# Optimization experiments

Measured on AMD Instinct MI355X. Metric: run time of the kernel, lower is better.

The kernel has to match this reference:

```python
import jax, jax.numpy as jnp
import numpy as np

HIDDEN = 1408
HEADS = 16
HEAD_DIM = 88  # HIDDEN // HEADS
NUM_PATCHES = 576  # (336 // 14) ** 2
SEQ = NUM_PATCHES + 1  # +1 CLS token position in mllama4 rope cache
ROPE_BASE = 10000.0
SCALE = HEAD_DIM ** -0.5


def _rope_cos_sin():
    # Faithful to vLLM Llama4VisionRotaryEmbedding cos/sin cache.
    idx = np.arange(NUM_PATCHES, dtype=np.int64).reshape(NUM_PATCHES, 1)
    idx = np.concatenate([idx, idx[:1]], axis=0)
    idx[-1, -1] = -2  # CLS token id -> zero rotation
    n = int(np.sqrt(NUM_PATCHES))  # patches per side = 24
    fx = idx % n
    fy = idx // n
    rd = HEAD_DIM // 2  # rotary_dim = 44
    inv = 1.0 / ROPE_BASE ** (np.arange(0, rd, 2, dtype=np.float32) / rd)  # (22,)
    # repeat_interleave(2) then cat then [::2] == concat of the two 22-d halves
    freqs = np.concatenate(
        [(fx + 1)[..., None] * inv[None, None, :], (fy + 1)[..., None] * inv[None, None, :]],
        axis=-1,
    )  # (SEQ, 1, 44)
    freqs = np.where(idx.reshape(-1, 1, 1) < 0, 0.0, freqs).astype(np.float32)
    freqs = freqs.squeeze(1)  # (SEQ, 44)
    return jnp.asarray(np.cos(freqs)), jnp.asarray(np.sin(freqs))


_COS, _SIN = _rope_cos_sin()


def _apply_rope(x, cos, sin):
    # x: [B, S, H, D]; complex rotation over adjacent pairs (is_neox_style=False)
    B, S, H, D = x.shape
    xp = x.reshape(B, S, H, D // 2, 2)
    x0, x1 = xp[..., 0], xp[..., 1]
    c = cos[None, :, None, :]  # [1, S, 1, D//2]
    s = sin[None, :, None, :]
    out = jnp.stack([x0 * c - x1 * s, x0 * s + x1 * c], axis=-1)
    return out.reshape(B, S, H, D)


def setup_inputs() -> dict:
    key = jax.random.key(0)
    k1, k2, k3, k4, k5 = jax.random.split(key, 5)
    std = HIDDEN ** -0.5
    return {
        "hidden_states": jax.random.normal(k1, (32, SEQ, HIDDEN), dtype=jnp.float32),
        "w_qkv": jax.random.normal(k2, (HIDDEN, 3 * HIDDEN), dtype=jnp.float32) * std,
        "b_qkv": jax.random.normal(k3, (3 * HIDDEN,), dtype=jnp.float32) * 0.02,
        "w_o": jax.random.normal(k4, (HIDDEN, HIDDEN), dtype=jnp.float32) * std,
        "b_o": jax.random.normal(k5, (HIDDEN,), dtype=jnp.float32) * 0.02,
    }


def reference(hidden_states, w_qkv, b_qkv, w_o, b_o):
    B, S, _ = hidden_states.shape
    qkv = hidden_states @ w_qkv + b_qkv  # [B, S, 3*HIDDEN]
    q, k, v = jnp.split(qkv, 3, axis=-1)
    q = q.reshape(B, S, HEADS, HEAD_DIM)
    k = k.reshape(B, S, HEADS, HEAD_DIM)
    v = v.reshape(B, S, HEADS, HEAD_DIM)
    q = _apply_rope(q, _COS, _SIN)
    k = _apply_rope(k, _COS, _SIN)
    scores = jnp.einsum("bqhd,bkhd->bhqk", q, k) * SCALE
    probs = jax.nn.softmax(scores, axis=-1)
    attn = jnp.einsum("bhqk,bkhd->bqhd", probs, v).reshape(B, S, HIDDEN)
    return attn @ w_o + b_o
```

## Files before the change

### kernel.cpp

```cpp
#include <hip/hip_runtime.h>
#include <math.h>

#define HEADS    16
#define HEAD_DIM 88
#define SEQ      577
#define SEQV     640
#define HIDDEN   1408
#define NQKV     4224
#define NQKV_PAD 4352
#define NOUT_PAD 1536
#define RD       44
#define SCALE_F  0.1066003581778052f
#define MPAD_ROWS 18688
#define NKT      22
#define BUF_SH   32768

typedef __attribute__((ext_vector_type(8))) short bf16x8;
typedef __attribute__((ext_vector_type(4))) float f32x4;

__device__ __forceinline__ unsigned short f2bf(float x) {
    unsigned u = __float_as_uint(x);
    unsigned r = u + 0x7fff + ((u >> 16) & 1);
    return (unsigned short)(r >> 16);
}
__device__ __forceinline__ f32x4 fzero() {
    f32x4 z; z.x = 0.f; z.y = 0.f; z.z = 0.f; z.w = 0.f; return z;
}
__device__ __forceinline__ int xcd_swz(int flat, int nwg) {
    int q = nwg >> 3, r = nwg & 7;
    int x = flat & 7, j = flat >> 3;
    return (x < r ? x * (q + 1) : r * (q + 1) + (x - r) * q) + j;
}

__global__ void rope_precompute(float* __restrict__ cosb, float* __restrict__ sinb) {
    int s = blockIdx.x;
    int j = threadIdx.x;
    if (j >= RD) return;
    float c, sn;
    if (s == SEQ - 1) {
        c = 1.f; sn = 0.f;
    } else {
        int fx = s % 24, fy = s / 24;
        int p = (j < 22) ? j : j - 22;
        float inv = powf(10000.f, -(float)p / 22.f);
        float f = (float)((j < 22 ? fx : fy) + 1) * inv;
        c = cosf(f); sn = sinf(f);
    }
    cosb[s * RD + j] = c;
    sinb[s * RD + j] = sn;
}

__global__ void conv_hs(const float* __restrict__ in, unsigned short* __restrict__ out,
                        long nreal, long ntot) {
    long i = ((long)blockIdx.x * 256 + threadIdx.x) * 4;
    if (i >= ntot) return;
    ushort4 o;
    if (i < nreal) {
        float4 v = *(const float4*)(in + i);
        o = make_ushort4(f2bf(v.x), f2bf(v.y), f2bf(v.z), f2bf(v.w));
    } else {
        o = make_ushort4(0, 0, 0, 0);
    }
    *(ushort4*)(out + i) = o;
}

__global__ void conv_wT(const float* __restrict__ in, unsigned short* __restrict__ out,
                        int R, int Creal) {
    __shared__ float t[32][33];
    int bx = blockIdx.x * 32, by = blockIdx.y * 32;
    int tx = threadIdx.x & 31, ty = threadIdx.x >> 5;
    #pragma unroll
    for (int i = 0; i < 4; ++i) {
        int col = bx + tx;
        t[ty + i * 8][tx] = (col < Creal) ? in[(size_t)(by + ty + i * 8) * Creal + col] : 0.f;
    }
    __syncthreads();
    #pragma unroll
    for (int i = 0; i < 4; ++i)
        out[(size_t)(bx + ty + i * 8) * R + by + tx] = f2bf(t[tx][ty + i * 8]);
}

__device__ __forceinline__ void stage_half(const unsigned short* __restrict__ src,
                                           int kt, unsigned short* lds, int tid) {
    #pragma unroll
    for (int q = 0; q < 2; ++q) {
        int cf = tid + 512 * q;
        int r  = cf >> 3, c = cf & 7;
        int cg = c ^ (r & 7);
        __builtin_amdgcn_global_load_lds(
            (const __attribute__((address_space(1))) void*)(src + (size_t)r * HIDDEN + kt * 64 + cg * 8),
            (__attribute__((address_space(3))) void*)(lds + cf * 8),
            16, 0, 0);
    }
}

template<int N> __device__ __forceinline__ void vwait() {
    if constexpr (N >= 0)
        asm volatile("s_waitcnt vmcnt(%0)" :: "i"(N) : "memory");
}

template<int CBUF, int IH, int JH, bool STG, int SSIDE, int SHALF, int SBUF, int WAITN>
__device__ __forceinline__ void phase8(
    const unsigned short* __restrict__ wsrc, const unsigned short* __restrict__ hsrc,
    unsigned short* smem, int skt, int tid,
    int ww, int wh, int quad, int l15, f32x4 (&acc)[8][4])
{
    bf16x8 afr[4][2], bfr[2][2];
    #pragma unroll
    for (int i2 = 0; i2 < 4; ++i2)
        #pragma unroll
        for (int kk = 0; kk < 2; ++kk) {
            int r = ww * 64 + i2 * 16 + l15;
            afr[i2][kk] = *(const bf16x8*)(smem + CBUF * BUF_SH + IH * 8192
                          + r * 64 + (((kk * 4 + quad) ^ (r & 7)) << 3));
        }
    #pragma unroll
    for (int j2 = 0; j2 < 2; ++j2)
        #pragma unroll
        for (int kk = 0; kk < 2; ++kk) {
            int r = wh * 32 + j2 * 16 + l15;
            bfr[j2][kk] = *(const bf16x8*)(smem + CBUF * BUF_SH + 16384 + JH * 8192
                          + r * 64 + (((kk * 4 + quad) ^ (r & 7)) << 3));
        }
    if constexpr (STG) {
        const unsigned short* s = (SSIDE ? hsrc : wsrc) + (size_t)SHALF * 128 * HIDDEN;
        stage_half(s, skt, smem + SBUF * BUF_SH + (SSIDE ? 16384 : 0) + SHALF * 8192, tid);
    }
    __builtin_amdgcn_sched_barrier(0);
    __builtin_amdgcn_s_barrier();
    __builtin_amdgcn_sched_barrier(0);
    __builtin_amdgcn_s_setprio(1);
    #pragma unroll
    for (int i2 = 0; i2 < 4; ++i2)
        #pragma unroll
        for (int j2 = 0; j2 < 2; ++j2)
            #pragma unroll
            for (int kk = 0; kk < 2; ++kk)
                acc[IH * 4 + i2][JH * 2 + j2] = __builtin_amdgcn_mfma_f32_16x16x32_bf16(
                    afr[i2][kk], bfr[j2][kk], acc[IH * 4 + i2][JH * 2 + j2], 0, 0, 0);
    __builtin_amdgcn_s_setprio(0);
    __builtin_amdgcn_sched_barrier(0);
    vwait<WAITN>();
    __builtin_amdgcn_s_barrier();
    __builtin_amdgcn_sched_barrier(0);
}

__device__ __forceinline__ void gemm256_8ph(
    const unsigned short* __restrict__ wsrc, const unsigned short* __restrict__ hsrc,
    unsigned short* smem, int tid, f32x4 (&acc)[8][4])
{
    const int lane = tid & 63, w8 = tid >> 6;
    const int quad = lane >> 4, l15 = lane & 15;
    const int ww = w8 >> 2, wh = w8 & 3;

    stage_half(wsrc,                0, smem,                  tid);
    stage_half(hsrc,                0, smem + 16384,          tid);
    stage_half(wsrc + 128 * HIDDEN, 0, smem + 8192,           tid);
    stage_half(hsrc + 128 * HIDDEN, 0, smem + 24576,          tid);
    stage_half(wsrc,                1, smem + BUF_SH,         tid);
    stage_half(hsrc,                1, smem + BUF_SH + 16384, tid);
    asm volatile("s_waitcnt vmcnt(4)" ::: "memory");
    __builtin_amdgcn_s_barrier();
    __builtin_amdgcn_sched_barrier(0);

    for (int it = 0; it < 10; ++it) {
        int k1 = 2 * it + 1, k2 = 2 * it + 2, k3 = 2 * it + 3;
        phase8<0,0,0, true,0,1,1,  6>(wsrc, hsrc, smem, k1, tid, ww, wh, quad, l15, acc);
        phase8<0,0,1, true,1,1,1, -1>(wsrc, hsrc, smem, k1, tid, ww, wh, quad, l15, acc);
        phase8<0,1,0, true,0,0,0, -1>(wsrc, hsrc, smem, k2, tid, ww, wh, quad, l15, acc);
        phase8<0,1,1, true,1,0,0,  8>(wsrc, hsrc, smem, k2, tid, ww, wh, quad, l15, acc);
        phase8<1,0,0, true,0,1,0,  6>(wsrc, hsrc, smem, k2, tid, ww, wh, quad, l15, acc);
        phase8<1,0,1, true,1,1,0, -1>(wsrc, hsrc, smem, k2, tid, ww, wh, quad, l15, acc);
        phase8<1,1,0, true,0,0,1, -1>(wsrc, hsrc, smem, k3, tid, ww, wh, quad, l15, acc);
        phase8<1,1,1, true,1,0,1,  8>(wsrc, hsrc, smem, k3, tid, ww, wh, quad, l15, acc);
    }
    phase8<0,0,0, true,0,1,1,  6>(wsrc, hsrc, smem, 21, tid, ww, wh, quad, l15, acc);
    phase8<0,0,1, true,1,1,1, -1>(wsrc, hsrc, smem, 21, tid, ww, wh, quad, l15, acc);
    phase8<0,1,0, false,0,0,0, -1>(wsrc, hsrc, smem, 0, tid, ww, wh, quad, l15, acc);
    phase8<0,1,1, false,0,0,0,  4>(wsrc, hsrc, smem, 0, tid, ww, wh, quad, l15, acc);
    phase8<1,0,0, false,0,0,0,  0>(wsrc, hsrc, smem, 0, tid, ww, wh, quad, l15, acc);
    phase8<1,0,1, false,0,0,0, -1>(wsrc, hsrc, smem, 0, tid, ww, wh, quad, l15, acc);
    phase8<1,1,0, false,0,0,0, -1>(wsrc, hsrc, smem, 0, tid, ww, wh, quad, l15, acc);
    phase8<1,1,1, false,0,0,0, -1>(wsrc, hsrc, smem, 0, tid, ww, wh, quad, l15, acc);
}

__global__ __launch_bounds__(512, 2) void qkv_mfma(
    const unsigned short* __restrict__ hsb, const unsigned short* __restrict__ wt,
    const float* __restrict__ bias, const float* __restrict__ cosb,
    const float* __restrict__ sinb,
    unsigned short* __restrict__ qb, unsigned short* __restrict__ kb,
    unsigned short* __restrict__ vtb,
    int Mchunk, int row_off)
{
    __shared__ unsigned short smem[2 * BUF_SH];
    int tid = threadIdx.x;
    int lane = tid & 63, w8 = tid >> 6;
    int quad = lane >> 4, l15 = lane & 15;
    int ww = w8 >> 2, wh = w8 & 3;

    int nwg  = gridDim.x * gridDim.y;
    int flat = blockIdx.y * gridDim.x + blockIdx.x;
    int wg   = xcd_swz(flat, nwg);
    int n0   = (wg % gridDim.x) * 256;
    int m0   = (wg / gridDim.x) * 256;

    f32x4 acc[8][4];
    #pragma unroll
    for (int i = 0; i < 8; ++i)
        #pragma unroll
        for (int j = 0; j < 4; ++j) acc[i][j] = fzero();

    gemm256_8ph(wt + (size_t)n0 * HIDDEN,
                hsb + (size_t)(row_off + m0) * HIDDEN, smem, tid, acc);

    #pragma unroll
    for (int j = 0; j < 4; ++j) {
        int m = m0 + (j >> 1) * 128 + wh * 32 + (j & 1) * 16 + l15;
        if (m >= Mchunk) continue;
        int bb = m / SEQ;
        int s  = m - bb * SEQ;
        const float* cr = cosb + s * RD;
        const float* sr = sinb + s * RD;
        #pragma unroll
        for (int i = 0; i < 8; ++i) {
            int ng = n0 + (i >> 2) * 128 + ww * 64 + (i & 3) * 16 + quad * 4;
            if (ng >= NQKV) continue;
            int sec = ng / HIDDEN;
            int nn  = ng - sec * HIDDEN;
            int h   = nn / HEAD_DIM;
            int d0  = nn - h * HEAD_DIM;
            int bh  = bb * HEADS + h;
            f32x4 v = acc[i][j];
            const float4 bv = *(const float4*)(bias + ng);
            v.x += bv.x; v.y += bv.y; v.z += bv.z; v.w += bv.w;
            if (sec < 2) {
                int p0 = d0 >> 1;
                float c0 = cr[p0],     s0 = sr[p0];
                float c1 = cr[p0 + 1], s1 = sr[p0 + 1];
                float x0 = v.x, x1 = v.y;
                v.x = x0 * c0 - x1 * s0; v.y = x0 * s0 + x1 * c0;
                x0 = v.z; x1 = v.w;
                v.z = x0 * c1 - x1 * s1; v.w = x0 * s1 + x1 * c1;
                if (sec == 0) { v.x *= SCALE_F; v.y *= SCALE_F; v.z *= SCALE_F; v.w *= SCALE_F; }
                unsigned short* dst = (sec == 0) ? qb : kb;
                ushort4 o = make_ushort4(f2bf(v.x), f2bf(v.y), f2bf(v.z), f2bf(v.w));
                *(ushort4*)(dst + ((size_t)bh * SEQ + s) * HEAD_DIM + d0) = o;
            } else {
                unsigned short* vb = vtb + ((size_t)bh * HEAD_DIM + d0) * SEQV + s;
                vb[0]        = f2bf(v.x);
                vb[SEQV]     = f2bf(v.y);
                vb[2 * SEQV] = f2bf(v.z);
                vb[3 * SEQV] = f2bf(v.w);
            }
        }
    }
}

__global__ __launch_bounds__(512, 2) void out_mfma(
    const unsigned short* __restrict__ ab, const unsigned short* __restrict__ wt,
    const float* __restrict__ bias, float* __restrict__ out,
    int Mchunk, int row_off)
{
    __shared__ unsigned short smem[2 * BUF_SH];
    int tid = threadIdx.x;
    int lane = tid & 63, w8 = tid >> 6;
    int quad = lane >> 4, l15 = lane & 15;
    int ww = w8 >> 2, wh = w8 & 3;

    int nwg  = gridDim.x * gridDim.y;
    int flat = blockIdx.y * gridDim.x + blockIdx.x;
    int wg   = xcd_swz(flat, nwg);
    int n0   = (wg % gridDim.x) * 256;
    int m0   = (wg / gridDim.x) * 256;

    f32x4 acc[8][4];
    #pragma unroll
    for (int i = 0; i < 8; ++i)
        #pragma unroll
        for (int j = 0; j < 4; ++j) acc[i][j] = fzero();

    gemm256_8ph(wt + (size_t)n0 * HIDDEN,
                ab + (size_t)m0 * HIDDEN, smem, tid, acc);

    #pragma unroll
    for (int j = 0; j < 4; ++j) {
        int m = m0 + (j >> 1) * 128 + wh * 32 + (j & 1) * 16 + l15;
        if (m >= Mchunk) continue;
        size_t orow = (size_t)(row_off + m) * HIDDEN;
        #pragma unroll
        for (int i = 0; i < 8; ++i) {
            int nn = n0 + (i >> 2) * 128 + ww * 64 + (i & 3) * 16 + quad * 4;
            if (nn >= HIDDEN) continue;
            f32x4 v = acc[i][j];
            const float4 bv = *(const float4*)(bias + nn);
            v.x += bv.x; v.y += bv.y; v.z += bv.z; v.w += bv.w;
            *(f32x4*)(out + orow + nn) = v;
        }
    }
}

#define QT   128
#define KTT  64
#define PSTR 72
#define RESCALE_THR 8.0f

__global__ __launch_bounds__(256, 3) void attn_mfma(
    const unsigned short* __restrict__ qb, const unsigned short* __restrict__ kb,
    const unsigned short* __restrict__ vtb, unsigned short* __restrict__ awsb)
{
    __shared__ unsigned short Ps[QT * PSTR];

    int tid = threadIdx.x;
    int lane = tid & 63, wv = tid >> 6;
    int quad = lane >> 4, l15 = lane & 15;

    int nwg  = gridDim.x * gridDim.y * gridDim.z;
    int flat = (blockIdx.z * gridDim.y + blockIdx.y) * gridDim.x + blockIdx.x;
    int w    = xcd_swz(flat, nwg);
    int qblk = w % gridDim.x;
    int rem  = w / gridDim.x;
    int h    = rem % gridDim.y;
    int bb   = rem / gridDim.y;
    int q0   = qblk * QT;
    int bh   = bb * HEADS + h;
    const unsigned short* qg = qb  + (size_t)bh * SEQ * HEAD_DIM;
    const unsigned short* kg = kb  + (size_t)bh * SEQ * HEAD_DIM;
    const unsigned short* vg = vtb + (size_t)bh * HEAD_DIM * SEQV;

    bf16x8 qf[2][3];
    #pragma unroll
    for (int mf = 0; mf < 2; ++mf)
        #pragma unroll
        for (int ks = 0; ks < 3; ++ks)
            qf[mf][ks] = *(const bf16x8*)(qg +
                (size_t)(q0 + wv * 32 + mf * 16 + l15) * HEAD_DIM + ks * 32 + quad * 8);

    f32x4 O[2][6];
    float m_i[2], l_i[2];
    #pragma unroll
    for (int mf = 0; mf < 2; ++mf) {
        #pragma unroll
        for (int nf = 0; nf < 6; ++nf) O[mf][nf] = fzero();
        m_i[mf] = -INFINITY; l_i[mf] = 0.f;
    }

    for (int k0 = 0; k0 < SEQ; k0 += KTT) {
        bf16x8 kf[3][4];
        #pragma unroll
        for (int ks = 0; ks < 3; ++ks)
            #pragma unroll
            for (int nf = 0; nf < 4; ++nf) {
                bf16x8 v = *(const bf16x8*)(kg +
                    (size_t)(k0 + nf * 16 + l15) * HEAD_DIM + ks * 32 + quad * 8);
                if (ks == 2 && quad == 3) v = (bf16x8)(short)0;
                kf[ks][nf] = v;
            }

        f32x4 sc[2][4];
        #pragma unroll
        for (int mf = 0; mf < 2; ++mf)
            #pragma unroll
            for (int nf = 0; nf < 4; ++nf) sc[mf][nf] = fzero();
        __builtin_amdgcn_s_setprio(1);
        #pragma unroll
        for (int ks = 0; ks < 3; ++ks) {
            #pragma unroll
            for (int nf = 0; nf < 4; ++nf) {
                sc[0][nf] = __builtin_amdgcn_mfma_f32_16x16x32_bf16(kf[ks][nf], qf[0][ks], sc[0][nf], 0, 0, 0);
                sc[1][nf] = __builtin_amdgcn_mfma_f32_16x16x32_bf16(kf[ks][nf], qf[1][ks], sc[1][nf], 0, 0, 0);
            }
        }
        __builtin_amdgcn_s_setprio(0);

        bf16x8 vf[2][6];
        auto smx = [&](int mf) {
            float pmax = -INFINITY;
            #pragma unroll
            for (int nf = 0; nf < 4; ++nf)
                #pragma unroll
                for (int r = 0; r < 4; ++r)
                    if (k0 + nf * 16 + quad * 4 + r < SEQ)
                        pmax = fmaxf(pmax, sc[mf][nf][r]);
            pmax = fmaxf(pmax, __shfl_xor(pmax, 16));
            pmax = fmaxf(pmax, __shfl_xor(pmax, 32));
            float mold = m_i[mf];
            bool skip = __all(pmax - mold <= RESCALE_THR);
            float mnew = skip ? mold : fmaxf(mold, pmax);
            float rsum = 0.f;
            #pragma unroll
            for (int nf = 0; nf < 4; ++nf) {
                ushort4 o;
                #pragma unroll
                for (int r = 0; r < 4; ++r) {
                    bool valid = (k0 + nf * 16 + quad * 4 + r < SEQ);
                    float p = valid ? __expf(sc[mf][nf][r] - mnew) : 0.f;
                    rsum += p;
                    ((unsigned short*)&o)[r] = f2bf(p);
                }
                *(ushort4*)(Ps + (wv * 32 + mf * 16 + l15) * PSTR + nf * 16 + quad * 4) = o;
            }
            rsum += __shfl_xor(rsum, 16);
            rsum += __shfl_xor(rsum, 32);
            if (!skip) {
                float alpha = __expf(mold - mnew);
                m_i[mf] = mnew;
                l_i[mf] = l_i[mf] * alpha + rsum;
                #pragma unroll
                for (int r = 0; r < 4; ++r) {
                    float ar = __shfl(alpha, quad * 4 + r, 16);
                    #pragma unroll
                    for (int nf = 0; nf < 6; ++nf) O[mf][nf][r] *= ar;
                }
            } else {
                l_i[mf] += rsum;
            }
        };

        smx(0);
        #pragma unroll
        for (int ks = 0; ks < 2; ++ks)
            #pragma unroll
            for (int nf = 0; nf < 6; ++nf)
                vf[ks][nf] = *(const bf16x8*)(vg +
                    (size_t)(nf * 16 + l15) * SEQV + k0 + ks * 32 + quad * 8);
        smx(1);

        __builtin_amdgcn_s_setprio(1);
        #pragma unroll
        for (int ks = 0; ks < 2; ++ks) {
            bf16x8 a0 = *(const bf16x8*)(Ps + (wv * 32 + l15) * PSTR + ks * 32 + quad * 8);
            bf16x8 a1 = *(const bf16x8*)(Ps + (wv * 32 + 16 + l15) * PSTR + ks * 32 + quad * 8);
            #pragma unroll
            for (int nf = 0; nf < 6; ++nf) {
                O[0][nf] = __builtin_amdgcn_mfma_f32_16x16x32_bf16(a0, vf[ks][nf], O[0][nf], 0, 0, 0);
                O[1][nf] = __builtin_amdgcn_mfma_f32_16x16x32_bf16(a1, vf[ks][nf], O[1][nf], 0, 0, 0);
            }
        }
        __builtin_amdgcn_s_setprio(0);
    }

    #pragma unroll
    for (int mf = 0; mf < 2; ++mf) {
        #pragma unroll
        for (int r = 0; r < 4; ++r) {
            int row = q0 + wv * 32 + mf * 16 + quad * 4 + r;
            if (row >= SEQ) continue;
            float lb = __shfl(l_i[mf], quad * 4 + r, 16);
            float il = 1.f / lb;
            size_t base = (size_t)(bb * SEQ + row) * HIDDEN + h * HEAD_DIM;
            #pragma unroll
            for (int nf = 0; nf < 6; ++nf) {
                int d = nf * 16 + l15;
                if (d < HEAD_DIM)
                    awsb[base + d] = f2bf(O[mf][nf][r] * il);
            }
        }
    }
}

extern "C" void kernel_launch(void* const* d_in, const int* in_sizes, int n_in,
                              void* d_out, int out_size, void* d_ws, size_t ws_size,
                              hipStream_t stream) {
    const float* hs    = (const float*)d_in[0];
    const float* w_qkv = (const float*)d_in[1];
    const float* b_qkv = (const float*)d_in[2];
    const float* w_o   = (const float*)d_in[3];
    const float* b_o   = (const float*)d_in[4];
    float* out = (float*)d_out;

    char* p = (char*)d_ws;
    auto alloc = [&](size_t bytes) {
        char* r = p; p += (bytes + 255) & ~(size_t)255; return r;
    };
    float*          cosb   = (float*)alloc((size_t)SEQ * RD * 4);
    float*          sinb   = (float*)alloc((size_t)SEQ * RD * 4);
    unsigned short* wqkv_t = (unsigned short*)alloc((size_t)NQKV_PAD * HIDDEN * 2);
    unsigned short* wo_t   = (unsigned short*)alloc((size_t)NOUT_PAD * HIDDEN * 2);
    unsigned short* hs_bf  = (unsigned short*)alloc((size_t)MPAD_ROWS * HIDDEN * 2);
    size_t fixed = (size_t)(p - (char*)d_ws);

    size_t per_batch = 2ull * HEADS * SEQ * HEAD_DIM * 2
                     + (size_t)HEADS * HEAD_DIM * SEQV * 2
                     + (size_t)SEQ * HIDDEN * 2;
    size_t pads = 2ull * 128 * HEAD_DIM * 2 + 24ull * SEQV * 2 + 256ull * HIDDEN * 2 + 16 * 256;
    size_t rem = (ws_size > fixed + pads) ? ws_size - fixed - pads : 0;
    int CB = (int)(rem / per_batch);
    if (CB < 1) CB = 1;
    if (CB > 32) CB = 32;

    unsigned short* qbuf  = (unsigned short*)alloc(((size_t)CB * HEADS * SEQ + 128) * HEAD_DIM * 2);
    unsigned short* kbuf  = (unsigned short*)alloc(((size_t)CB * HEADS * SEQ + 128) * HEAD_DIM * 2);
    unsigned short* vtbuf = (unsigned short*)alloc(((size_t)CB * HEADS * HEAD_DIM + 24) * SEQV * 2);
    unsigned short* awsb  = (unsigned short*)alloc(((size_t)CB * SEQ + 256) * HIDDEN * 2);

    rope_precompute<<<dim3(SEQ), dim3(64), 0, stream>>>(cosb, sinb);

    long nreal = (long)32 * SEQ * HIDDEN;
    long ntot  = (long)MPAD_ROWS * HIDDEN;
    conv_hs<<<dim3((unsigned)((ntot / 4 + 255) / 256)), 256, 0, stream>>>(hs, hs_bf, nreal, ntot);
    conv_wT<<<dim3(NQKV_PAD / 32, HIDDEN / 32), 256, 0, stream>>>(w_qkv, wqkv_t, HIDDEN, NQKV);
    conv_wT<<<dim3(NOUT_PAD / 32, HIDDEN / 32), 256, 0, stream>>>(w_o, wo_t, HIDDEN, HIDDEN);

    for (int b_off = 0; b_off < 32; b_off += CB) {
        int nb = (32 - b_off < CB) ? (32 - b_off) : CB;
        int M = nb * SEQ;

        dim3 g1(NQKV_PAD / 256, (M + 255) / 256);
        qkv_mfma<<<g1, 512, 0, stream>>>(hs_bf, wqkv_t, b_qkv, cosb, sinb,
                                         qbuf, kbuf, vtbuf, M, b_off * SEQ);
        dim3 g2((SEQ + QT - 1) / QT, HEADS, nb);
        attn_mfma<<<g2, 256, 0, stream>>>(qbuf, kbuf, vtbuf, awsb);
        dim3 g3(NOUT_PAD / 256, (M + 255) / 256);
        out_mfma<<<g3, 512, 0, stream>>>(awsb, wo_t, b_o, out, M, b_off * SEQ);
    }
}
```

Baseline: 759.2 us.

## Use single-wave attention workgroups with 32-query tiles and peel masked tail

Each attention workgroup now holds one wavefront processing 32 query rows instead of four waves over 128 rows. The grid grows from 5 to 19 query blocks per head, which trims wasted work on the padded last query tile and gives the scheduler finer-grained blocks. The key loop is split into unmasked full tiles and a single masked final tile, so the bounds checks are dropped from the common path. The softmax max and sum reductions are also restructured into trees. The cost is more workgroups and less sharing of block-level resources.

```diff
diff --git a/kernel.cpp b/kernel.cpp
--- a/kernel.cpp
+++ b/kernel.cpp
@@ -299,19 +299,123 @@
     }
 }
 
-#define QT   128
 #define KTT  64
 #define PSTR 72
 #define RESCALE_THR 8.0f
 
-__global__ __launch_bounds__(256, 3) void attn_mfma(
+template<bool FULL>
+__device__ __forceinline__ void attn_step(
+    int k0, const unsigned short* __restrict__ kg, const unsigned short* __restrict__ vg,
+    unsigned short* __restrict__ Ps, int quad, int l15,
+    const bf16x8 (&qf)[2][3], f32x4 (&O)[2][6], float (&m_i)[2], float (&l_i)[2])
+{
+    bf16x8 kf[3][4];
+    #pragma unroll
+    for (int ks = 0; ks < 3; ++ks)
+        #pragma unroll
+        for (int nf = 0; nf < 4; ++nf) {
+            bf16x8 v = *(const bf16x8*)(kg +
+                (size_t)(k0 + nf * 16 + l15) * HEAD_DIM + ks * 32 + quad * 8);
+            if (ks == 2 && quad == 3) v = (bf16x8)(short)0;
+            kf[ks][nf] = v;
+        }
+
+    f32x4 sc[2][4];
+    #pragma unroll
+    for (int mf = 0; mf < 2; ++mf)
+        #pragma unroll
+        for (int nf = 0; nf < 4; ++nf) sc[mf][nf] = fzero();
+    __builtin_amdgcn_s_setprio(1);
+    #pragma unroll
+    for (int ks = 0; ks < 3; ++ks)
+        #pragma unroll
+        for (int nf = 0; nf < 4; ++nf) {
+            sc[0][nf] = __builtin_amdgcn_mfma_f32_16x16x32_bf16(kf[ks][nf], qf[0][ks], sc[0][nf], 0, 0, 0);
+            sc[1][nf] = __builtin_amdgcn_mfma_f32_16x16x32_bf16(kf[ks][nf], qf[1][ks], sc[1][nf], 0, 0, 0);
+        }
+    __builtin_amdgcn_s_setprio(0);
+
+    bf16x8 vf[2][6];
+    auto smx = [&](int mf) {
+        float t[4];
+        #pragma unroll
+        for (int nf = 0; nf < 4; ++nf) {
+            float mv[4];
+            #pragma unroll
+            for (int r = 0; r < 4; ++r) {
+                bool valid = FULL || (k0 + nf * 16 + quad * 4 + r < SEQ);
+                mv[r] = valid ? sc[mf][nf][r] : -INFINITY;
+            }
+            t[nf] = fmaxf(fmaxf(mv[0], mv[1]), fmaxf(mv[2], mv[3]));
+        }
+        float pmax = fmaxf(fmaxf(t[0], t[1]), fmaxf(t[2], t[3]));
+        pmax = fmaxf(pmax, __shfl_xor(pmax, 16));
+        pmax = fmaxf(pmax, __shfl_xor(pmax, 32));
+        float mold = m_i[mf];
+        bool skip = __all(pmax - mold <= RESCALE_THR);
+        float mnew = skip ? mold : fmaxf(mold, pmax);
+        float rsum = 0.f;
+        #pragma unroll
+        for (int nf = 0; nf < 4; ++nf) {
+            ushort4 o;
+            float s0 = 0.f, s1 = 0.f;
+            #pragma unroll
+            for (int r = 0; r < 4; ++r) {
+                bool valid = FULL || (k0 + nf * 16 + quad * 4 + r < SEQ);
+                float p = valid ? __expf(sc[mf][nf][r] - mnew) : 0.f;
+                if (r < 2) s0 += p; else s1 += p;
+                ((unsigned short*)&o)[r] = f2bf(p);
+            }
+            rsum += s0 + s1;
+            *(ushort4*)(Ps + (mf * 16 + l15) * PSTR + nf * 16 + quad * 4) = o;
+        }
+        rsum += __shfl_xor(rsum, 16);
+        rsum += __shfl_xor(rsum, 32);
+        if (!skip) {
+            float alpha = __expf(mold - mnew);
+            m_i[mf] = mnew;
+            l_i[mf] = l_i[mf] * alpha + rsum;
+            #pragma unroll
+            for (int r = 0; r < 4; ++r) {
+                float ar = __shfl(alpha, quad * 4 + r, 16);
+                #pragma unroll
+                for (int nf = 0; nf < 6; ++nf) O[mf][nf][r] *= ar;
+            }
+        } else {
+            l_i[mf] += rsum;
+        }
+    };
+
+    smx(0);
+    #pragma unroll
+    for (int ks = 0; ks < 2; ++ks)
+        #pragma unroll
+        for (int nf = 0; nf < 6; ++nf)
+            vf[ks][nf] = *(const bf16x8*)(vg +
+                (size_t)(nf * 16 + l15) * SEQV + k0 + ks * 32 + quad * 8);
+    smx(1);
+
+    __builtin_amdgcn_s_setprio(1);
+    #pragma unroll
+    for (int ks = 0; ks < 2; ++ks) {
+        bf16x8 a0 = *(const bf16x8*)(Ps + l15 * PSTR + ks * 32 + quad * 8);
+        bf16x8 a1 = *(const bf16x8*)(Ps + (16 + l15) * PSTR + ks * 32 + quad * 8);
+        #pragma unroll
+        for (int nf = 0; nf < 6; ++nf) {
+            O[0][nf] = __builtin_amdgcn_mfma_f32_16x16x32_bf16(a0, vf[ks][nf], O[0][nf], 0, 0, 0);
+            O[1][nf] = __builtin_amdgcn_mfma_f32_16x16x32_bf16(a1, vf[ks][nf], O[1][nf], 0, 0, 0);
+        }
+    }
+    __builtin_amdgcn_s_setprio(0);
+}
+
+__global__ __launch_bounds__(64, 3) void attn_mfma(
     const unsigned short* __restrict__ qb, const unsigned short* __restrict__ kb,
     const unsigned short* __restrict__ vtb, unsigned short* __restrict__ awsb)
 {
-    __shared__ unsigned short Ps[QT * PSTR];
-
-    int tid = threadIdx.x;
-    int lane = tid & 63, wv = tid >> 6;
+    __shared__ unsigned short Ps[32 * PSTR];
+
+    int lane = threadIdx.x;
     int quad = lane >> 4, l15 = lane & 15;
 
     int nwg  = gridDim.x * gridDim.y * gridDim.z;
@@ -321,7 +425,7 @@
     int rem  = w / gridDim.x;
     int h    = rem % gridDim.y;
     int bb   = rem / gridDim.y;
-    int q0   = qblk * QT;
+    int q0   = qblk * 32;
     int bh   = bb * HEADS + h;
     const unsigned short* qg = qb  + (size_t)bh * SEQ * HEAD_DIM;
     const unsigned short* kg = kb  + (size_t)bh * SEQ * HEAD_DIM;
@@ -333,7 +437,7 @@
         #pragma unroll
         for (int ks = 0; ks < 3; ++ks)
             qf[mf][ks] = *(const bf16x8*)(qg +
-                (size_t)(q0 + wv * 32 + mf * 16 + l15) * HEAD_DIM + ks * 32 + quad * 8);
+                (size_t)(q0 + mf * 16 + l15) * HEAD_DIM + ks * 32 + quad * 8);
 
     f32x4 O[2][6];
     float m_i[2], l_i[2];
@@ -344,106 +448,15 @@
         m_i[mf] = -INFINITY; l_i[mf] = 0.f;
     }
 
-    for (int k0 = 0; k0 < SEQ; k0 += KTT) {
-        bf16x8 kf[3][4];
-        #pragma unroll
-        for (int ks = 0; ks < 3; ++ks)
-            #pragma unroll
-            for (int nf = 0; nf < 4; ++nf) {
-                bf16x8 v = *(const bf16x8*)(kg +
-                    (size_t)(k0 + nf * 16 + l15) * HEAD_DIM + ks * 32 + quad * 8);
-                if (ks == 2 && quad == 3) v = (bf16x8)(short)0;
-                kf[ks][nf] = v;
-            }
-
-        f32x4 sc[2][4];
-        #pragma unroll
-        for (int mf = 0; mf < 2; ++mf)
-            #pragma unroll
-            for (int nf = 0; nf < 4; ++nf) sc[mf][nf] = fzero();
-        __builtin_amdgcn_s_setprio(1);
-        #pragma unroll
-        for (int ks = 0; ks < 3; ++ks) {
-            #pragma unroll
-            for (int nf = 0; nf < 4; ++nf) {
-                sc[0][nf] = __builtin_amdgcn_mfma_f32_16x16x32_bf16(kf[ks][nf], qf[0][ks], sc[0][nf], 0, 0, 0);
-                sc[1][nf] = __builtin_amdgcn_mfma_f32_16x16x32_bf16(kf[ks][nf], qf[1][ks], sc[1][nf], 0, 0, 0);
-            }
-        }
-        __builtin_amdgcn_s_setprio(0);
-
-        bf16x8 vf[2][6];
-        auto smx = [&](int mf) {
-            float pmax = -INFINITY;
-            #pragma unroll
-            for (int nf = 0; nf < 4; ++nf)
-                #pragma unroll
-                for (int r = 0; r < 4; ++r)
-                    if (k0 + nf * 16 + quad * 4 + r < SEQ)
-                        pmax = fmaxf(pmax, sc[mf][nf][r]);
-            pmax = fmaxf(pmax, __shfl_xor(pmax, 16));
-            pmax = fmaxf(pmax, __shfl_xor(pmax, 32));
-            float mold = m_i[mf];
-            bool skip = __all(pmax - mold <= RESCALE_THR);
-            float mnew = skip ? mold : fmaxf(mold, pmax);
-            float rsum = 0.f;
-            #pragma unroll
-            for (int nf = 0; nf < 4; ++nf) {
-                ushort4 o;
-                #pragma unroll
-                for (int r = 0; r < 4; ++r) {
-                    bool valid = (k0 + nf * 16 + quad * 4 + r < SEQ);
-                    float p = valid ? __expf(sc[mf][nf][r] - mnew) : 0.f;
-                    rsum += p;
-                    ((unsigned short*)&o)[r] = f2bf(p);
-                }
-                *(ushort4*)(Ps + (wv * 32 + mf * 16 + l15) * PSTR + nf * 16 + quad * 4) = o;
-            }
-            rsum += __shfl_xor(rsum, 16);
-            rsum += __shfl_xor(rsum, 32);
-            if (!skip) {
-                float alpha = __expf(mold - mnew);
-                m_i[mf] = mnew;
-                l_i[mf] = l_i[mf] * alpha + rsum;
-                #pragma unroll
-                for (int r = 0; r < 4; ++r) {
-                    float ar = __shfl(alpha, quad * 4 + r, 16);
-                    #pragma unroll
-                    for (int nf = 0; nf < 6; ++nf) O[mf][nf][r] *= ar;
-                }
-            } else {
-                l_i[mf] += rsum;
-            }
-        };
-
-        smx(0);
-        #pragma unroll
-        for (int ks = 0; ks < 2; ++ks)
-            #pragma unroll
-            for (int nf = 0; nf < 6; ++nf)
-                vf[ks][nf] = *(const bf16x8*)(vg +
-                    (size_t)(nf * 16 + l15) * SEQV + k0 + ks * 32 + quad * 8);
-        smx(1);
-
-        __builtin_amdgcn_s_setprio(1);
-        #pragma unroll
-        for (int ks = 0; ks < 2; ++ks) {
-            bf16x8 a0 = *(const bf16x8*)(Ps + (wv * 32 + l15) * PSTR + ks * 32 + quad * 8);
-            bf16x8 a1 = *(const bf16x8*)(Ps + (wv * 32 + 16 + l15) * PSTR + ks * 32 + quad * 8);
-            #pragma unroll
-            for (int nf = 0; nf < 6; ++nf) {
-                O[0][nf] = __builtin_amdgcn_mfma_f32_16x16x32_bf16(a0, vf[ks][nf], O[0][nf], 0, 0, 0);
-                O[1][nf] = __builtin_amdgcn_mfma_f32_16x16x32_bf16(a1, vf[ks][nf], O[1][nf], 0, 0, 0);
-            }
-        }
-        __builtin_amdgcn_s_setprio(0);
-    }
+    for (int k0 = 0; k0 < SEQ - KTT; k0 += KTT)
+        attn_step<true>(k0, kg, vg, Ps, quad, l15, qf, O, m_i, l_i);
+    attn_step<false>(576, kg, vg, Ps, quad, l15, qf, O, m_i, l_i);
 
     #pragma unroll
     for (int mf = 0; mf < 2; ++mf) {
         #pragma unroll
         for (int r = 0; r < 4; ++r) {
-            int row = q0 + wv * 32 + mf * 16 + quad * 4 + r;
+            int row = q0 + mf * 16 + quad * 4 + r;
             if (row >= SEQ) continue;
             float lb = __shfl(l_i[mf], quad * 4 + r, 16);
             float il = 1.f / lb;
@@ -508,8 +521,8 @@
         dim3 g1(NQKV_PAD / 256, (M + 255) / 256);
         qkv_mfma<<<g1, 512, 0, stream>>>(hs_bf, wqkv_t, b_qkv, cosb, sinb,
                                          qbuf, kbuf, vtbuf, M, b_off * SEQ);
-        dim3 g2((SEQ + QT - 1) / QT, HEADS, nb);
-        attn_mfma<<<g2, 256, 0, stream>>>(qbuf, kbuf, vtbuf, awsb);
+        dim3 g2((SEQ + 31) / 32, HEADS, nb);
+        attn_mfma<<<g2, 64, 0, stream>>>(qbuf, kbuf, vtbuf, awsb);
         dim3 g3(NOUT_PAD / 256, (M + 255) / 256);
         out_mfma<<<g3, 512, 0, stream>>>(awsb, wo_t, b_o, out, M, b_off * SEQ);
     }
```

Result: no change. 760.4 us (+0.2%).
